# Kernel optimization log

Measured on AMD Instinct MI355X. Metric: run time of the kernel, lower is better.

Reference implementation:

```python
import jax, jax.numpy as jnp
import numpy as np

MARGIN = 0.7
ITERS = 1000  # as hard-coded in ot_loss's log_optimal_transport call


def setup_inputs() -> dict:
    key = jax.random.key(0)
    k1, k2 = jax.random.split(key)
    # features: N x C x W x H  (query at index 0, 8 targets)
    x = jax.random.normal(k1, (9, 256, 32, 32), dtype=jnp.float32)
    # attention: N x W x H, strictly positive since it is logged directly
    att = jax.random.uniform(k2, (9, 32, 32), dtype=jnp.float32, minval=0.1, maxval=1.0)
    return {"x": x, "att": att, "label": 1}


def _ot_distance(x, att):
    N, C, W, H = x.shape
    m = W * H              # number of query locations
    n = (N - 1) * W * H    # number of target locations
    Q = x[0].reshape(C, m).T                                          # (m, C)
    T = x[1:].reshape(N - 1, C, m).transpose(0, 2, 1).reshape(n, C)   # (n, C)
    mu = att[0].reshape(m)      # query marginal
    nu = att[1:].reshape(n)     # target marginal
    # pairwise squared euclidean distances (m, n)
    M = (jnp.sum(Q * Q, axis=1)[:, None]
         + jnp.sum(T * T, axis=1)[None, :]
         - 2.0 * (Q @ T.T))
    log_mu = jnp.log(mu)
    log_nu = jnp.log(nu)

    def step(carry, _):
        u, v = carry
        u = log_mu - jax.nn.logsumexp(M + v[None, :], axis=1)
        v = log_nu - jax.nn.logsumexp(M + u[:, None], axis=0)
        return (u, v), None

    init = (jnp.zeros((m,), M.dtype), jnp.zeros((n,), M.dtype))
    (u, v), _ = jax.lax.scan(jax.checkpoint(step), init, None, length=ITERS)
    P = jnp.exp(M + u[:, None] + v[None, :])   # transport plan (m, n)
    # OT barycentric distance per query location, summed
    diff = mu[:, None] * Q - P @ T             # (m, C)
    return jnp.sqrt(jnp.sum(diff * diff, axis=1)).sum()


def reference(x, att, label):
    d = _ot_distance(x, att)
    if label:  # label is a concrete python int: positive pair
        return d
    return jnp.clip(MARGIN - d, 0.0, None)
```

## Files before the change

### kernel.cpp

```cpp
#include <hip/hip_runtime.h>
#include <math.h>

#define MR 1024
#define NC 8192
#define NCH 256
#define OT_ITERS 1000
#define IMG_STRIDE 262144

__device__ inline float wredMax(float v){
#pragma unroll
  for (int m = 32; m >= 1; m >>= 1) v = fmaxf(v, __shfl_xor(v, m, 64));
  return v;
}
__device__ inline float wredMin(float v){
#pragma unroll
  for (int m = 32; m >= 1; m >>= 1) v = fminf(v, __shfl_xor(v, m, 64));
  return v;
}
__device__ inline float wredSum(float v){
#pragma unroll
  for (int m = 32; m >= 1; m >>= 1) v += __shfl_xor(v, m, 64);
  return v;
}

__device__ inline unsigned fkey(float f){
  unsigned b = __float_as_uint(f);
  return (b & 0x80000000u) ? ~b : (b | 0x80000000u);
}
__device__ inline float funkey(unsigned k){
  return (k & 0x80000000u) ? __uint_as_float(k & 0x7fffffffu) : __uint_as_float(~k);
}

__global__ __launch_bounds__(256) void kPrep(const float* __restrict__ x,
                                             const float* __restrict__ att,
                                             float* __restrict__ qq, float* __restrict__ tt,
                                             float* __restrict__ logmu, float* __restrict__ lognu,
                                             float* __restrict__ u, float* __restrict__ v,
                                             float* __restrict__ acc, unsigned* __restrict__ prmI){
  int idx = blockIdx.x * 256 + threadIdx.x;
  if (idx < 9216){
    int img = idx >> 10, pos = idx & 1023;
    const float* p = x + img * IMG_STRIDE + pos;
    float s = 0.f;
#pragma unroll 8
    for (int c = 0; c < NCH; ++c){ float a = p[c * 1024]; s += a * a; }
    float lg = logf(att[idx]);
    if (img == 0){ qq[idx] = s;        logmu[idx] = lg; }
    else         { tt[idx - 1024] = s; lognu[idx - 1024] = lg; }
  }
  if (idx < MR) u[idx] = 0.f;
  if (idx < NC) v[idx] = 0.f;
  if (idx == 0){ *acc = 0.f; prmI[0] = 0xFFFFFFFFu; prmI[1] = 0u; }
}

__global__ __launch_bounds__(256) void kGemmM(const float* __restrict__ x,
                                              const float* __restrict__ qq,
                                              const float* __restrict__ tt,
                                              float* __restrict__ M,
                                              unsigned* __restrict__ prmI){
  __shared__ float As[16][68];
  __shared__ float Bs[16][68];
  __shared__ float smn[4], smx[4];
  int jb = blockIdx.x;
  int ib = blockIdx.y;
  int i0 = ib * 64;
  int j0 = jb * 64;
  int k  = j0 >> 10, p0 = j0 & 1023;
  const float* A = x + i0;
  const float* B = x + (1 + k) * IMG_STRIDE + p0;
  int tid = threadIdx.x;
  int lr = tid >> 4, lc = (tid & 15) * 4;
  int ty = tid >> 4, tx = tid & 15;
  float accv[4][4] = {};
  for (int kt = 0; kt < 16; ++kt){
    int c = kt * 16 + lr;
    float4 av = *(const float4*)(A + c * 1024 + lc);
    float4 bv = *(const float4*)(B + c * 1024 + lc);
    *(float4*)(&As[lr][lc]) = av;
    *(float4*)(&Bs[lr][lc]) = bv;
    __syncthreads();
#pragma unroll
    for (int kk = 0; kk < 16; ++kk){
      float4 a = *(const float4*)(&As[kk][ty * 4]);
      float4 b = *(const float4*)(&Bs[kk][tx * 4]);
      float ar[4] = {a.x, a.y, a.z, a.w};
      float br[4] = {b.x, b.y, b.z, b.w};
#pragma unroll
      for (int r = 0; r < 4; ++r)
#pragma unroll
        for (int cc = 0; cc < 4; ++cc) accv[r][cc] += ar[r] * br[cc];
    }
    __syncthreads();
  }
  float tmn = INFINITY, tmx = -INFINITY;
#pragma unroll
  for (int r = 0; r < 4; ++r){
    int i = i0 + ty * 4 + r;
    float qi = qq[i];
    float o[4];
#pragma unroll
    for (int cc = 0; cc < 4; ++cc){
      o[cc] = qi + tt[j0 + tx * 4 + cc] - 2.f * accv[r][cc];
      tmn = fminf(tmn, o[cc]); tmx = fmaxf(tmx, o[cc]);
    }
    float4 ov = { o[0], o[1], o[2], o[3] };
    *(float4*)(M + (long)i * NC + j0 + tx * 4) = ov;
  }
  int lane = tid & 63, w = tid >> 6;
  tmn = wredMin(tmn); tmx = wredMax(tmx);
  if (lane == 0){ smn[w] = tmn; smx[w] = tmx; }
  __syncthreads();
  if (tid == 0){
    float bmn = fminf(fminf(smn[0], smn[1]), fminf(smn[2], smn[3]));
    float bmx = fmaxf(fmaxf(smx[0], smx[1]), fmaxf(smx[2], smx[3]));
    atomicMin(&prmI[0], fkey(bmn));
    atomicMax(&prmI[1], fkey(bmx));
  }
}

__global__ __launch_bounds__(256) void kQuantTrans(const float* __restrict__ M,
                                                   unsigned short* __restrict__ Mq,
                                                   unsigned short* __restrict__ Mtq,
                                                   float* __restrict__ prm){
  __shared__ float tile[64][65];
  const unsigned* prmI = (const unsigned*)prm;
  float mn = funkey(prmI[0]);
  float mx = funkey(prmI[1]);
  float rng = mx - mn;
  float inv = (rng > 0.f) ? 65535.0f / rng : 0.f;
  float sc  = (rng > 0.f) ? rng / 65535.0f : 0.f;
  int i0 = blockIdx.y * 64;
  int j0 = blockIdx.x * 64;
  int t = threadIdx.x;
  int tc = t & 63, tr = t >> 6;
#pragma unroll
  for (int rr = 0; rr < 64; rr += 4)
    tile[rr + tr][tc] = M[(long)(i0 + rr + tr) * NC + j0 + tc];
  __syncthreads();
#pragma unroll
  for (int rr = 0; rr < 64; rr += 4){
    float a = tile[rr + tr][tc];
    int qa = (int)lrintf((a - mn) * inv);
    qa = qa < 0 ? 0 : (qa > 65535 ? 65535 : qa);
    Mq[(long)(i0 + rr + tr) * NC + j0 + tc] = (unsigned short)qa;
    float b = tile[tc][rr + tr];
    int qb = (int)lrintf((b - mn) * inv);
    qb = qb < 0 ? 0 : (qb > 65535 ? 65535 : qb);
    Mtq[(long)(j0 + rr + tr) * MR + i0 + tc] = (unsigned short)qb;
  }
  if (blockIdx.x == 0 && blockIdx.y == 0 && t == 0){ prm[2] = mn; prm[3] = sc; }
}

__global__ __launch_bounds__(256) void kUPassQ(const unsigned short* __restrict__ Mq,
                                               const float* __restrict__ v,
                                               const float* __restrict__ logmu,
                                               float* __restrict__ u,
                                               const float* __restrict__ prm){
  int b = blockIdx.x, tid = threadIdx.x;
  float mn = prm[2], s = prm[3];
  int r0 = 2 * b;
  const unsigned short* R0 = Mq + (long)r0 * NC;
  const unsigned short* R1 = R0 + NC;
  float t0[32], t1[32];
  float mx0 = -INFINITY, mx1 = -INFINITY;
#pragma unroll
  for (int kb = 0; kb < 4; ++kb){
    int cidx = kb * 2048 + tid * 8;
    uint4 qa = *(const uint4*)(R0 + cidx);
    uint4 qb = *(const uint4*)(R1 + cidx);
    float4 v0 = *(const float4*)(v + cidx);
    float4 v1 = *(const float4*)(v + cidx + 4);
    float a0 = fmaf(s, (float)(qa.x & 0xFFFFu), v0.x);
    float a1 = fmaf(s, (float)(qa.x >> 16),     v0.y);
    float a2 = fmaf(s, (float)(qa.y & 0xFFFFu), v0.z);
    float a3 = fmaf(s, (float)(qa.y >> 16),     v0.w);
    float a4 = fmaf(s, (float)(qa.z & 0xFFFFu), v1.x);
    float a5 = fmaf(s, (float)(qa.z >> 16),     v1.y);
    float a6 = fmaf(s, (float)(qa.w & 0xFFFFu), v1.z);
    float a7 = fmaf(s, (float)(qa.w >> 16),     v1.w);
    float c0 = fmaf(s, (float)(qb.x & 0xFFFFu), v0.x);
    float c1 = fmaf(s, (float)(qb.x >> 16),     v0.y);
    float c2 = fmaf(s, (float)(qb.y & 0xFFFFu), v0.z);
    float c3 = fmaf(s, (float)(qb.y >> 16),     v0.w);
    float c4 = fmaf(s, (float)(qb.z & 0xFFFFu), v1.x);
    float c5 = fmaf(s, (float)(qb.z >> 16),     v1.y);
    float c6 = fmaf(s, (float)(qb.w & 0xFFFFu), v1.z);
    float c7 = fmaf(s, (float)(qb.w >> 16),     v1.w);
    t0[kb*8+0]=a0; t0[kb*8+1]=a1; t0[kb*8+2]=a2; t0[kb*8+3]=a3;
    t0[kb*8+4]=a4; t0[kb*8+5]=a5; t0[kb*8+6]=a6; t0[kb*8+7]=a7;
    t1[kb*8+0]=c0; t1[kb*8+1]=c1; t1[kb*8+2]=c2; t1[kb*8+3]=c3;
    t1[kb*8+4]=c4; t1[kb*8+5]=c5; t1[kb*8+6]=c6; t1[kb*8+7]=c7;
    mx0 = fmaxf(mx0, fmaxf(fmaxf(fmaxf(a0,a1),fmaxf(a2,a3)), fmaxf(fmaxf(a4,a5),fmaxf(a6,a7))));
    mx1 = fmaxf(mx1, fmaxf(fmaxf(fmaxf(c0,c1),fmaxf(c2,c3)), fmaxf(fmaxf(c4,c5),fmaxf(c6,c7))));
  }
  __shared__ float redA0[4], redA1[4], redB0[4], redB1[4];
  int lane = tid & 63, w = tid >> 6;
  float wm0 = wredMax(mx0), wm1 = wredMax(mx1);
  if (lane == 0){ redA0[w] = wm0; redA1[w] = wm1; }
  __syncthreads();
  float bm0 = fmaxf(fmaxf(redA0[0], redA0[1]), fmaxf(redA0[2], redA0[3]));
  float bm1 = fmaxf(fmaxf(redA1[0], redA1[1]), fmaxf(redA1[2], redA1[3]));
  float s0 = 0.f, s1 = 0.f;
#pragma unroll
  for (int q = 0; q < 32; ++q){ s0 += __expf(t0[q] - bm0); s1 += __expf(t1[q] - bm1); }
  s0 = wredSum(s0); s1 = wredSum(s1);
  if (lane == 0){ redB0[w] = s0; redB1[w] = s1; }
  __syncthreads();
  if (tid == 0){
    u[r0]     = logmu[r0]     - mn - (bm0 + __logf(redB0[0] + redB0[1] + redB0[2] + redB0[3]));
    u[r0 + 1] = logmu[r0 + 1] - mn - (bm1 + __logf(redB1[0] + redB1[1] + redB1[2] + redB1[3]));
  }
}

__global__ __launch_bounds__(256) void kVPassQ(const unsigned short* __restrict__ Mtq,
                                               const float* __restrict__ u,
                                               const float* __restrict__ lognu,
                                               float* __restrict__ v,
                                               const float* __restrict__ prm){
  __shared__ float ulds[1024];
  int tid = threadIdx.x;
  float mn = prm[2], s = prm[3];
  *(float4*)(&ulds[tid * 4]) = *(const float4*)(u + tid * 4);
  __syncthreads();
  int w = tid >> 6, lane = tid & 63;
#pragma unroll
  for (int cc = 0; cc < 4; ++cc){
    int j = blockIdx.x * 16 + w * 4 + cc;
    const unsigned short* R = Mtq + (long)j * MR;
    uint4 qa = *(const uint4*)(R + lane * 8);
    uint4 qb = *(const uint4*)(R + 512 + lane * 8);
    float4 ua0 = *(const float4*)(&ulds[lane * 8]);
    float4 ua1 = *(const float4*)(&ulds[lane * 8 + 4]);
    float4 ub0 = *(const float4*)(&ulds[512 + lane * 8]);
    float4 ub1 = *(const float4*)(&ulds[512 + lane * 8 + 4]);
    float tv[16];
    tv[0]  = fmaf(s, (float)(qa.x & 0xFFFFu), ua0.x);
    tv[1]  = fmaf(s, (float)(qa.x >> 16),     ua0.y);
    tv[2]  = fmaf(s, (float)(qa.y & 0xFFFFu), ua0.z);
    tv[3]  = fmaf(s, (float)(qa.y >> 16),     ua0.w);
    tv[4]  = fmaf(s, (float)(qa.z & 0xFFFFu), ua1.x);
    tv[5]  = fmaf(s, (float)(qa.z >> 16),     ua1.y);
    tv[6]  = fmaf(s, (float)(qa.w & 0xFFFFu), ua1.z);
    tv[7]  = fmaf(s, (float)(qa.w >> 16),     ua1.w);
    tv[8]  = fmaf(s, (float)(qb.x & 0xFFFFu), ub0.x);
    tv[9]  = fmaf(s, (float)(qb.x >> 16),     ub0.y);
    tv[10] = fmaf(s, (float)(qb.y & 0xFFFFu), ub0.z);
    tv[11] = fmaf(s, (float)(qb.y >> 16),     ub0.w);
    tv[12] = fmaf(s, (float)(qb.z & 0xFFFFu), ub1.x);
    tv[13] = fmaf(s, (float)(qb.z >> 16),     ub1.y);
    tv[14] = fmaf(s, (float)(qb.w & 0xFFFFu), ub1.z);
    tv[15] = fmaf(s, (float)(qb.w >> 16),     ub1.w);
    float mx = -INFINITY;
#pragma unroll
    for (int q = 0; q < 16; ++q) mx = fmaxf(mx, tv[q]);
    mx = wredMax(mx);
    float sm = 0.f;
#pragma unroll
    for (int q = 0; q < 16; ++q) sm += __expf(tv[q] - mx);
    sm = wredSum(sm);
    if (lane == 0) v[j] = lognu[j] - mn - (mx + __logf(sm));
  }
}

__global__ __launch_bounds__(256) void kFinal(const float* __restrict__ x,
                                              const float* __restrict__ att,
                                              const float* __restrict__ M,
                                              const float* __restrict__ u,
                                              const float* __restrict__ v,
                                              float* __restrict__ acc){
  __shared__ float pch[4][256];
  __shared__ float redS[4];
  int tid = threadIdx.x;
  int r0 = blockIdx.x * 4;
  float u4[4];
#pragma unroll
  for (int rr = 0; rr < 4; ++rr) u4[rr] = u[r0 + rr];
  float o[4] = {0.f, 0.f, 0.f, 0.f};
  for (int jc = 0; jc < NC; jc += 256){
    float vv = v[jc + tid];
#pragma unroll
    for (int rr = 0; rr < 4; ++rr)
      pch[rr][tid] = __expf(M[(long)(r0 + rr) * NC + jc + tid] + u4[rr] + vv);
    __syncthreads();
    int k = jc >> 10;
    const float* Tp = x + (1 + k) * IMG_STRIDE + tid * 1024 + (jc & 1023);
    for (int jj = 0; jj < 256; jj += 4){
      float4 tv = *(const float4*)(Tp + jj);
      float tq[4] = {tv.x, tv.y, tv.z, tv.w};
#pragma unroll
      for (int q = 0; q < 4; ++q){
        o[0] += pch[0][jj + q] * tq[q];
        o[1] += pch[1][jj + q] * tq[q];
        o[2] += pch[2][jj + q] * tq[q];
        o[3] += pch[3][jj + q] * tq[q];
      }
    }
    __syncthreads();
  }
  int lane = tid & 63, wid = tid >> 6;
  float dtot = 0.f;
#pragma unroll
  for (int rr = 0; rr < 4; ++rr){
    float mu = att[r0 + rr];
    float qv = x[tid * 1024 + (r0 + rr)];
    float diff = mu * qv - o[rr];
    float wsum = wredSum(diff * diff);
    if (lane == 0) redS[wid] = wsum;
    __syncthreads();
    if (tid == 0) dtot += sqrtf(redS[0] + redS[1] + redS[2] + redS[3]);
    __syncthreads();
  }
  if (tid == 0) atomicAdd(acc, dtot);
}

__global__ void kOut(const float* __restrict__ acc, const int* __restrict__ label,
                     float* __restrict__ out){
  if (threadIdx.x == 0 && blockIdx.x == 0){
    float d = *acc;
    out[0] = (*label) ? d : fmaxf(0.7f - d, 0.f);
  }
}

extern "C" void kernel_launch(void* const* d_in, const int* in_sizes, int n_in,
                              void* d_out, int out_size, void* d_ws, size_t ws_size,
                              hipStream_t stream){
  const float* x   = (const float*)d_in[0];
  const float* att = (const float*)d_in[1];
  const int* label = (const int*)d_in[2];
  float* W = (float*)d_ws;
  float* out = (float*)d_out;

  float* M = W;
  unsigned short* Mq  = (unsigned short*)(W + 8388608);
  unsigned short* Mtq = (unsigned short*)(W + 8388608 + 4194304);
  float* S     = W + 16777216;
  float* qq    = S;
  float* tt    = qq + 1024;
  float* logmu = tt + 8192;
  float* lognu = logmu + 1024;
  float* u     = lognu + 8192;
  float* v     = u + 1024;
  float* acc   = v + 8192;
  float* prm   = acc + 1;
  unsigned* prmI = (unsigned*)prm;

  hipLaunchKernelGGL(kPrep, dim3(37), dim3(256), 0, stream, x, att, qq, tt, logmu, lognu, u, v, acc, prmI);
  hipLaunchKernelGGL(kGemmM, dim3(128, 16), dim3(256), 0, stream, x, qq, tt, M, prmI);
  hipLaunchKernelGGL(kQuantTrans, dim3(128, 16), dim3(256), 0, stream, M, Mq, Mtq, prm);
  for (int it = 0; it < OT_ITERS; ++it){
    hipLaunchKernelGGL(kUPassQ, dim3(512), dim3(256), 0, stream, Mq, v, logmu, u, prm);
    hipLaunchKernelGGL(kVPassQ, dim3(512), dim3(256), 0, stream, Mtq, u, lognu, v, prm);
  }
  hipLaunchKernelGGL(kFinal, dim3(256), dim3(256), 0, stream, x, att, M, u, v, acc);
  hipLaunchKernelGGL(kOut, dim3(1), dim3(1), 0, stream, acc, label, out);
}
```

Baseline: 12.50 ms.

## Fuse Sinkhorn iterations into one persistent cooperative kernel with grid barriers

Replaces the 2000 separate kernel launches for the u and v passes with a single persistent cooperative kernel of 256 blocks. A custom epoch-based grid barrier built on cache-bypassing loads and atomic stores separates the passes. Each block stages v or u in shared memory and uses exp2/log2 with prescaled inputs. This is meant to remove per-launch overhead and idle gaps between launches. In exchange it adds spin-wait barrier cost, needs every block co-resident, and keeps the old launch loop as a fallback if the cooperative launch fails.

New measurement: 21.88 ms. +75.1%, slower.

```diff
diff --git a/kernel.cpp b/kernel.cpp
--- a/kernel.cpp
+++ b/kernel.cpp
@@ -6,6 +6,9 @@
 #define NCH 256
 #define OT_ITERS 1000
 #define IMG_STRIDE 262144
+#define PBLK 256
+#define L2EF 1.44269504088896340736f
+#define LN2F 0.69314718055994530942f
 
 __device__ inline float wredMax(float v){
 #pragma unroll
@@ -20,6 +23,11 @@
 __device__ inline float wredSum(float v){
 #pragma unroll
   for (int m = 32; m >= 1; m >>= 1) v += __shfl_xor(v, m, 64);
+  return v;
+}
+__device__ inline int wredMinI(int v){
+#pragma unroll
+  for (int m = 32; m >= 1; m >>= 1) v = min(v, __shfl_xor(v, m, 64));
   return v;
 }
 
@@ -29,6 +37,27 @@
 }
 __device__ inline float funkey(unsigned k){
   return (k & 0x80000000u) ? __uint_as_float(k & 0x7fffffffu) : __uint_as_float(~k);
+}
+
+__device__ inline float4 cload_f4(const float4* p){
+  float4 r;
+  asm volatile("global_load_dwordx4 %0, %1, off sc0 sc1\n\ts_waitcnt vmcnt(0)"
+               : "=v"(r) : "v"(p) : "memory");
+  return r;
+}
+__device__ inline void cload_f4x4(float4* r, const float4* p){
+  asm volatile(
+    "global_load_dwordx4 %0, %4, off sc0 sc1\n\t"
+    "global_load_dwordx4 %1, %5, off sc0 sc1\n\t"
+    "global_load_dwordx4 %2, %6, off sc0 sc1\n\t"
+    "global_load_dwordx4 %3, %7, off sc0 sc1\n\t"
+    "s_waitcnt vmcnt(0)"
+    : "=&v"(r[0]), "=&v"(r[1]), "=&v"(r[2]), "=v"(r[3])
+    : "v"(p), "v"(p + 1), "v"(p + 2), "v"(p + 3)
+    : "memory");
+}
+__device__ inline void astore(float* p, float val){
+  __hip_atomic_store(p, val, __ATOMIC_RELAXED, __HIP_MEMORY_SCOPE_AGENT);
 }
 
 __global__ __launch_bounds__(256) void kPrep(const float* __restrict__ x,
@@ -36,7 +65,8 @@
                                              float* __restrict__ qq, float* __restrict__ tt,
                                              float* __restrict__ logmu, float* __restrict__ lognu,
                                              float* __restrict__ u, float* __restrict__ v,
-                                             float* __restrict__ acc, unsigned* __restrict__ prmI){
+                                             float* __restrict__ acc, unsigned* __restrict__ prmI,
+                                             int* __restrict__ bar){
   int idx = blockIdx.x * 256 + threadIdx.x;
   if (idx < 9216){
     int img = idx >> 10, pos = idx & 1023;
@@ -50,6 +80,7 @@
   }
   if (idx < MR) u[idx] = 0.f;
   if (idx < NC) v[idx] = 0.f;
+  if (idx < 1024) bar[idx] = 0;
   if (idx == 0){ *acc = 0.f; prmI[0] = 0xFFFFFFFFu; prmI[1] = 0u; }
 }
 
@@ -149,6 +180,163 @@
     Mtq[(long)(j0 + rr + tr) * MR + i0 + tc] = (unsigned short)qb;
   }
   if (blockIdx.x == 0 && blockIdx.y == 0 && t == 0){ prm[2] = mn; prm[3] = sc; }
+}
+
+__device__ inline void gbar2(int* slots, int b, int ep){
+  __syncthreads();
+  if (threadIdx.x < 64){
+    int lane = threadIdx.x;
+    if (lane == 0){
+      asm volatile("s_waitcnt vmcnt(0)" ::: "memory");
+      __hip_atomic_store(&slots[b], ep, __ATOMIC_RELAXED, __HIP_MEMORY_SCOPE_AGENT);
+    }
+    const float4* p = (const float4*)slots + lane;
+    for (;;){
+      float4 s4 = cload_f4(p);
+      int m0 = min(min(__float_as_int(s4.x), __float_as_int(s4.y)),
+                   min(__float_as_int(s4.z), __float_as_int(s4.w)));
+      if (wredMinI(m0) >= ep) break;
+      __builtin_amdgcn_s_sleep(2);
+    }
+  }
+  __syncthreads();
+}
+
+__global__ __launch_bounds__(512) void kSink5(const unsigned short* __restrict__ Mq,
+                                              const unsigned short* __restrict__ Mtq,
+                                              const float* __restrict__ logmu,
+                                              const float* __restrict__ lognu,
+                                              float* __restrict__ u,
+                                              float* __restrict__ v,
+                                              const float* __restrict__ prm,
+                                              int* __restrict__ bar){
+  __shared__ float vsh[8192];
+  __shared__ float ush[1024];
+  __shared__ float redA[8], redB[8];
+  int tid = threadIdx.x, b = blockIdx.x;
+  int lane = tid & 63, w = tid >> 6;
+  float mn = prm[2], s = prm[3];
+  float s2 = s * L2EF;
+  int r0 = 4 * b;
+  int jb0 = 32 * b + 4 * w;
+  float lmu[4];
+#pragma unroll
+  for (int r = 0; r < 4; ++r) lmu[r] = logmu[r0 + r];
+  float lnu4[4];
+#pragma unroll
+  for (int cc = 0; cc < 4; ++cc) lnu4[cc] = lognu[jb0 + cc];
+  int ep = 0;
+
+  for (int it = 0; it < OT_ITERS; ++it){
+    {
+      float4 vb[4];
+      cload_f4x4(vb, (const float4*)v + 4 * tid);
+      float4* d = (float4*)&vsh[16 * tid];
+#pragma unroll
+      for (int k = 0; k < 4; ++k){
+        vb[k].x *= L2EF; vb[k].y *= L2EF; vb[k].z *= L2EF; vb[k].w *= L2EF;
+        d[k] = vb[k];
+      }
+    }
+    __syncthreads();
+
+#pragma unroll
+    for (int r = 0; r < 4; ++r){
+      const unsigned short* Rr = Mq + (long)(r0 + r) * NC + 16 * tid;
+      uint4 qa = *(const uint4*)(Rr);
+      uint4 qb = *(const uint4*)(Rr + 8);
+      const float* vp = &vsh[16 * tid];
+      float4 v0 = *(const float4*)(vp);
+      float4 v1 = *(const float4*)(vp + 4);
+      float4 v2 = *(const float4*)(vp + 8);
+      float4 v3 = *(const float4*)(vp + 12);
+      float tv[16];
+      tv[0]  = fmaf(s2, (float)(qa.x & 0xFFFFu), v0.x);
+      tv[1]  = fmaf(s2, (float)(qa.x >> 16),     v0.y);
+      tv[2]  = fmaf(s2, (float)(qa.y & 0xFFFFu), v0.z);
+      tv[3]  = fmaf(s2, (float)(qa.y >> 16),     v0.w);
+      tv[4]  = fmaf(s2, (float)(qa.z & 0xFFFFu), v1.x);
+      tv[5]  = fmaf(s2, (float)(qa.z >> 16),     v1.y);
+      tv[6]  = fmaf(s2, (float)(qa.w & 0xFFFFu), v1.z);
+      tv[7]  = fmaf(s2, (float)(qa.w >> 16),     v1.w);
+      tv[8]  = fmaf(s2, (float)(qb.x & 0xFFFFu), v2.x);
+      tv[9]  = fmaf(s2, (float)(qb.x >> 16),     v2.y);
+      tv[10] = fmaf(s2, (float)(qb.y & 0xFFFFu), v2.z);
+      tv[11] = fmaf(s2, (float)(qb.y >> 16),     v2.w);
+      tv[12] = fmaf(s2, (float)(qb.z & 0xFFFFu), v3.x);
+      tv[13] = fmaf(s2, (float)(qb.z >> 16),     v3.y);
+      tv[14] = fmaf(s2, (float)(qb.w & 0xFFFFu), v3.z);
+      tv[15] = fmaf(s2, (float)(qb.w >> 16),     v3.w);
+      float mx = -INFINITY;
+#pragma unroll
+      for (int q = 0; q < 16; ++q) mx = fmaxf(mx, tv[q]);
+      mx = wredMax(mx);
+      if (lane == 0) redA[w] = mx;
+      __syncthreads();
+      float bmx = fmaxf(fmaxf(fmaxf(redA[0], redA[1]), fmaxf(redA[2], redA[3])),
+                        fmaxf(fmaxf(redA[4], redA[5]), fmaxf(redA[6], redA[7])));
+      float sm = 0.f;
+#pragma unroll
+      for (int q = 0; q < 16; ++q) sm += __builtin_exp2f(tv[q] - bmx);
+      sm = wredSum(sm);
+      if (lane == 0) redB[w] = sm;
+      __syncthreads();
+      if (tid == 0){
+        float tot = ((redB[0] + redB[1]) + (redB[2] + redB[3]))
+                  + ((redB[4] + redB[5]) + (redB[6] + redB[7]));
+        astore(u + r0 + r, lmu[r] - mn - (bmx + __builtin_log2f(tot)) * LN2F);
+      }
+      __syncthreads();
+    }
+    gbar2(bar, b, ++ep);
+
+    if (tid < 256){
+      float4 uu = cload_f4((const float4*)u + tid);
+      uu.x *= L2EF; uu.y *= L2EF; uu.z *= L2EF; uu.w *= L2EF;
+      *(float4*)&ush[4 * tid] = uu;
+    }
+    __syncthreads();
+
+#pragma unroll
+    for (int cc = 0; cc < 4; ++cc){
+      int j = jb0 + cc;
+      const unsigned short* Rc = Mtq + (long)j * MR + 16 * lane;
+      uint4 qa = *(const uint4*)(Rc);
+      uint4 qb = *(const uint4*)(Rc + 8);
+      const float* up = &ush[16 * lane];
+      float4 u0 = *(const float4*)(up);
+      float4 u1 = *(const float4*)(up + 4);
+      float4 u2 = *(const float4*)(up + 8);
+      float4 u3 = *(const float4*)(up + 12);
+      float tv[16];
+      tv[0]  = fmaf(s2, (float)(qa.x & 0xFFFFu), u0.x);
+      tv[1]  = fmaf(s2, (float)(qa.x >> 16),     u0.y);
+      tv[2]  = fmaf(s2, (float)(qa.y & 0xFFFFu), u0.z);
+      tv[3]  = fmaf(s2, (float)(qa.y >> 16),     u0.w);
+      tv[4]  = fmaf(s2, (float)(qa.z & 0xFFFFu), u1.x);
+      tv[5]  = fmaf(s2, (float)(qa.z >> 16),     u1.y);
+      tv[6]  = fmaf(s2, (float)(qa.w & 0xFFFFu), u1.z);
+      tv[7]  = fmaf(s2, (float)(qa.w >> 16),     u1.w);
+      tv[8]  = fmaf(s2, (float)(qb.x & 0xFFFFu), u2.x);
+      tv[9]  = fmaf(s2, (float)(qb.x >> 16),     u2.y);
+      tv[10] = fmaf(s2, (float)(qb.y & 0xFFFFu), u2.z);
+      tv[11] = fmaf(s2, (float)(qb.y >> 16),     u2.w);
+      tv[12] = fmaf(s2, (float)(qb.z & 0xFFFFu), u3.x);
+      tv[13] = fmaf(s2, (float)(qb.z >> 16),     u3.y);
+      tv[14] = fmaf(s2, (float)(qb.w & 0xFFFFu), u3.z);
+      tv[15] = fmaf(s2, (float)(qb.w >> 16),     u3.w);
+      float mx = -INFINITY;
+#pragma unroll
+      for (int q = 0; q < 16; ++q) mx = fmaxf(mx, tv[q]);
+      mx = wredMax(mx);
+      float sm = 0.f;
+#pragma unroll
+      for (int q = 0; q < 16; ++q) sm += __builtin_exp2f(tv[q] - mx);
+      sm = wredSum(sm);
+      if (lane == 0) astore(v + j, lnu4[cc] - mn - (mx + __builtin_log2f(sm)) * LN2F);
+    }
+    gbar2(bar, b, ++ep);
+  }
 }
 
 __global__ __launch_bounds__(256) void kUPassQ(const unsigned short* __restrict__ Mq,
@@ -335,21 +523,29 @@
   unsigned short* Mtq = (unsigned short*)(W + 8388608 + 4194304);
   float* S     = W + 16777216;
   float* qq    = S;
-  float* tt    = qq + 1024;
-  float* logmu = tt + 8192;
-  float* lognu = logmu + 1024;
-  float* u     = lognu + 8192;
-  float* v     = u + 1024;
-  float* acc   = v + 8192;
-  float* prm   = acc + 1;
+  float* tt    = S + 1024;
+  float* logmu = S + 9216;
+  float* lognu = S + 10240;
+  float* u     = S + 18432;
+  float* v     = S + 19456;
+  float* acc   = S + 27648;
+  float* prm   = S + 27652;
   unsigned* prmI = (unsigned*)prm;
-
-  hipLaunchKernelGGL(kPrep, dim3(37), dim3(256), 0, stream, x, att, qq, tt, logmu, lognu, u, v, acc, prmI);
+  int*   bar   = (int*)(S + 27664);
+
+  hipLaunchKernelGGL(kPrep, dim3(37), dim3(256), 0, stream, x, att, qq, tt, logmu, lognu, u, v, acc, prmI, bar);
   hipLaunchKernelGGL(kGemmM, dim3(128, 16), dim3(256), 0, stream, x, qq, tt, M, prmI);
   hipLaunchKernelGGL(kQuantTrans, dim3(128, 16), dim3(256), 0, stream, M, Mq, Mtq, prm);
-  for (int it = 0; it < OT_ITERS; ++it){
-    hipLaunchKernelGGL(kUPassQ, dim3(512), dim3(256), 0, stream, Mq, v, logmu, u, prm);
-    hipLaunchKernelGGL(kVPassQ, dim3(512), dim3(256), 0, stream, Mtq, u, lognu, v, prm);
+
+  void* args[] = { (void*)&Mq, (void*)&Mtq, (void*)&logmu, (void*)&lognu,
+                   (void*)&u, (void*)&v, (void*)&prm, (void*)&bar };
+  hipError_t rc = hipLaunchCooperativeKernel((const void*)kSink5,
+                                             dim3(PBLK), dim3(512), args, 0, stream);
+  if (rc != hipSuccess){
+    for (int it = 0; it < OT_ITERS; ++it){
+      hipLaunchKernelGGL(kUPassQ, dim3(512), dim3(256), 0, stream, Mq, v, logmu, u, prm);
+      hipLaunchKernelGGL(kVPassQ, dim3(512), dim3(256), 0, stream, Mtq, u, lognu, v, prm);
+    }
   }
   hipLaunchKernelGGL(kFinal, dim3(256), dim3(256), 0, stream, x, att, M, u, v, acc);
   hipLaunchKernelGGL(kOut, dim3(1), dim3(1), 0, stream, acc, label, out);
```
